# Optimization experiments

Hardware: AMD Instinct MI355X
Metric: run time of the kernel (lower is better)

Reference implementation:

```python
import jax, jax.numpy as jnp
import numpy as np

D = 1024      # input_dim == output_dim
H = 512       # expert_dim
E = 8         # num_experts
TOP_K = 2
LN_EPS = 1e-5


def setup_inputs() -> dict:
    key = jax.random.key(0)
    ks = jax.random.split(key, 9)
    s_in = 1.0 / np.sqrt(D)
    s_h = 1.0 / np.sqrt(H)
    return {
        "x": jax.random.normal(ks[0], (4, 4096, D), dtype=jnp.float32),
        "Wg": jax.random.uniform(ks[1], (D, E), jnp.float32, -s_in, s_in),
        "bg": jax.random.uniform(ks[2], (E,), jnp.float32, -s_in, s_in),
        "W1": jax.random.uniform(ks[3], (E, D, H), jnp.float32, -s_in, s_in),
        "b1": jax.random.uniform(ks[4], (E, H), jnp.float32, -s_in, s_in),
        "W2": jax.random.uniform(ks[5], (E, H, D), jnp.float32, -s_h, s_h),
        "b2": jax.random.uniform(ks[6], (E, D), jnp.float32, -s_h, s_h),
        "gamma": jnp.ones((E, D), jnp.float32),
        "beta": jnp.zeros((E, D), jnp.float32),
    }


def reference(x, Wg, bg, W1, b1, W2, b2, gamma, beta):
    B, S, _ = x.shape
    xf = x.reshape(-1, D)                                   # [T, D]
    T = xf.shape[0]

    # Router (eval mode: no noise). Softmax over the top-k logits only.
    gates = xf @ Wg + bg                                    # [T, E]
    topw, topi = jax.lax.top_k(gates, TOP_K)                # [T, K]
    topw = jax.nn.softmax(topw, axis=-1)
    # Dense combine weights [T, E] (top_k indices are distinct per token).
    combine = jnp.zeros((T, E), xf.dtype).at[
        jnp.arange(T)[:, None], topi].add(topw)

    # All experts applied densely, combined with sparse routing weights
    # (same math as the masked gather/scatter loop in the original).
    h = jax.nn.gelu(jnp.einsum('td,edh->teh', xf, W1) + b1,
                    approximate=False)                      # [T, E, H]
    y = jnp.einsum('teh,ehd->ted', h, W2) + b2 + xf[:, None, :]  # residual
    mu = jnp.mean(y, axis=-1, keepdims=True)
    var = jnp.mean(jnp.square(y - mu), axis=-1, keepdims=True)
    yn = (y - mu) * jax.lax.rsqrt(var + LN_EPS) * gamma + beta   # per-expert LN

    out = jnp.einsum('te,ted->td', combine, yn)             # weighted combine
    return out.reshape(B, S, D)
```

## Files before the change

kernel.cpp:

```cpp
#include <hip/hip_runtime.h>

#define TT 16384
#define DD 1024
#define HH 512
#define EE 8
#define NA (2*TT)
#define NBLK (NA/256)
#define SLOT_CAP (NA + EE*128)
#define MT_TILES (SLOT_CAP/128)

typedef __attribute__((ext_vector_type(4))) float f32x4;
typedef __attribute__((ext_vector_type(8))) short s16x8;

__device__ __forceinline__ unsigned short f2bf(float f) {
  unsigned u = __float_as_uint(f);
  return (unsigned short)((u + 0x7fffu + ((u >> 16) & 1u)) >> 16);
}
__device__ __forceinline__ float bf2f(unsigned short h) {
  return __uint_as_float(((unsigned)h) << 16);
}
__device__ __forceinline__ float gelu_fast(float v) {
  float z = 1.5957691216057308f * (v + 0.044715f * v * v * v);
  return v / (1.0f + __expf(-z));
}
__device__ __forceinline__ void gl_lds16(const unsigned short* g, unsigned short* l) {
  __builtin_amdgcn_global_load_lds(
      (const __attribute__((address_space(1))) void*)g,
      (__attribute__((address_space(3))) void*)l, 16, 0, 0);
}


__global__ __launch_bounds__(256) void k_transpose(
    const float* __restrict__ src, unsigned short* __restrict__ dst, int R, int C) {
  __shared__ float t[32][33];
  const int e = blockIdx.z;
  const float* S = src + (size_t)e * R * C;
  unsigned short* Dt = dst + (size_t)e * R * C;
  const int c0 = blockIdx.x * 32, r0 = blockIdx.y * 32;
  const int tx = threadIdx.x & 31, ty = threadIdx.x >> 5;
#pragma unroll
  for (int i = 0; i < 4; i++)
    t[ty + i * 8][tx] = S[(size_t)(r0 + ty + i * 8) * C + c0 + tx];
  __syncthreads();
#pragma unroll
  for (int i = 0; i < 4; i++)
    Dt[(size_t)(c0 + ty + i * 8) * R + r0 + tx] = f2bf(t[tx][ty + i * 8]);
}

__global__ __launch_bounds__(256) void k_wgt(const float* __restrict__ Wg,
                                             float* __restrict__ WgT) {
  __shared__ float lds[DD * EE];
  const int tid = threadIdx.x;
#pragma unroll
  for (int k = 0; k < 32; k++) lds[tid + 256 * k] = Wg[tid + 256 * k];
  __syncthreads();
#pragma unroll
  for (int k = 0; k < 32; k++) {
    int f = tid + 256 * k;
    WgT[f] = lds[(f & 1023) * 8 + (f >> 10)];
  }
}

__global__ __launch_bounds__(256) void k_router(
    const float* __restrict__ x, const float* __restrict__ WgT,
    const float* __restrict__ bg, int* __restrict__ tok_e,
    float* __restrict__ tok_w, unsigned short* __restrict__ xbf) {
  const int lane = threadIdx.x & 63, wid = threadIdx.x >> 6;
  const int t = blockIdx.x * 4 + wid;
  const float4* xr4 = (const float4*)(x + (size_t)t * DD);
  ushort4* xb4 = (ushort4*)(xbf + (size_t)t * DD);
  float4 xv[4];
#pragma unroll
  for (int i = 0; i < 4; i++) {
    xv[i] = xr4[i * 64 + lane];
    ushort4 h;
    h.x = f2bf(xv[i].x); h.y = f2bf(xv[i].y);
    h.z = f2bf(xv[i].z); h.w = f2bf(xv[i].w);
    xb4[i * 64 + lane] = h;
  }
  float g[8];
#pragma unroll
  for (int e = 0; e < 8; e++) {
    const float4* w4 = (const float4*)(WgT + (size_t)e * DD);
    float a = 0.f;
#pragma unroll
    for (int i = 0; i < 4; i++) {
      float4 wv = w4[i * 64 + lane];
      a += xv[i].x * wv.x + xv[i].y * wv.y + xv[i].z * wv.z + xv[i].w * wv.w;
    }
    g[e] = a;
  }
#pragma unroll
  for (int off = 32; off; off >>= 1)
#pragma unroll
    for (int e2 = 0; e2 < 8; e2++) g[e2] += __shfl_xor(g[e2], off);
  if (lane == 0) {
#pragma unroll
    for (int e2 = 0; e2 < 8; e2++) g[e2] += bg[e2];
    int e1 = 0;
#pragma unroll
    for (int e2 = 1; e2 < 8; e2++) if (g[e2] > g[e1]) e1 = e2;
    int es = (e1 == 0) ? 1 : 0;
#pragma unroll
    for (int e2 = 0; e2 < 8; e2++) if (e2 != e1 && g[e2] > g[es]) es = e2;
    float p2 = expf(g[es] - g[e1]);
    float invs = 1.0f / (1.0f + p2);
    tok_e[2 * t] = e1; tok_e[2 * t + 1] = es;
    tok_w[2 * t] = invs; tok_w[2 * t + 1] = p2 * invs;
  }
}

__global__ __launch_bounds__(256) void k_hist(
    const int* __restrict__ tok_e, int* __restrict__ lrank,
    int* __restrict__ blockHist) {
  __shared__ int waveCnt[4][8];
  __shared__ int waveBase[4][8];
  const int tid = threadIdx.x, lane = tid & 63, wid = tid >> 6;
  const int i = blockIdx.x * 256 + tid;
  const int e = tok_e[i];
  int rw = 0;
#pragma unroll
  for (int ex = 0; ex < 8; ex++) {
    unsigned long long m = __ballot(e == ex);
    if (e == ex) rw = __popcll(m & ((1ull << lane) - 1ull));
    if (lane == 0) waveCnt[wid][ex] = __popcll(m);
  }
  __syncthreads();
  if (tid < 8) {
    int a0 = waveCnt[0][tid], a1 = waveCnt[1][tid];
    int a2 = waveCnt[2][tid], a3 = waveCnt[3][tid];
    waveBase[0][tid] = 0;
    waveBase[1][tid] = a0;
    waveBase[2][tid] = a0 + a1;
    waveBase[3][tid] = a0 + a1 + a2;
    blockHist[blockIdx.x * 8 + tid] = a0 + a1 + a2 + a3;
  }
  __syncthreads();
  lrank[i] = waveBase[wid][e] + rw;
}

__global__ __launch_bounds__(512) void k_scan(
    const int* __restrict__ blockHist, int* __restrict__ blockBase,
    int* __restrict__ offs) {
  __shared__ int tot[8];
  const int e = threadIdx.x >> 6;
  const int lane = threadIdx.x & 63;
  int v0 = blockHist[lane * 8 + e];
  int v1 = blockHist[(64 + lane) * 8 + e];
  int s0 = v0, s1 = v1;
#pragma unroll
  for (int off = 1; off < 64; off <<= 1) {
    int u0 = __shfl_up(s0, off), u1 = __shfl_up(s1, off);
    if (lane >= off) { s0 += u0; s1 += u1; }
  }
  int t0 = __shfl(s0, 63);
  blockBase[lane * 8 + e] = s0 - v0;
  blockBase[(64 + lane) * 8 + e] = t0 + s1 - v1;
  if (lane == 63) tot[e] = t0 + s1;
  __syncthreads();
  if (threadIdx.x == 0) {
    int acc = 0;
    offs[0] = 0;
#pragma unroll
    for (int e2 = 0; e2 < 8; e2++) {
      acc += (tot[e2] + 127) & ~127;
      offs[e2 + 1] = acc;
    }
  }
}

__global__ __launch_bounds__(256) void k_slotinit(int* __restrict__ st, int n) {
  int i = blockIdx.x * 256 + threadIdx.x;
  if (i < n) st[i] = 0;
}

__global__ __launch_bounds__(256) void k_assign(
    const int* __restrict__ tok_e, const int* __restrict__ lrank,
    const int* __restrict__ blockBase, const int* __restrict__ offs,
    int* __restrict__ slot_token, int* __restrict__ token_slot) {
  const int i = blockIdx.x * 256 + threadIdx.x;
  const int e = tok_e[i];
  const int slot = offs[e] + blockBase[blockIdx.x * 8 + e] + lrank[i];
  slot_token[slot] = i >> 1;
  token_slot[i] = slot;
}

template <int K, bool GATHER, int EPI, int NOUT>
__global__ __launch_bounds__(256, 2) void k_gemm(
    const unsigned short* __restrict__ A, const unsigned short* __restrict__ Bt,
    const int* __restrict__ offs, const int* __restrict__ slot_token,
    const float* __restrict__ bias, const unsigned short* __restrict__ xres,
    unsigned short* __restrict__ Out) {
  __shared__ unsigned short sA[128 * 64];
  __shared__ unsigned short sB[128 * 64];
  constexpr int NCT = NOUT / 128;
  constexpr int NWG = MT_TILES * NCT;
  constexpr int CPX = NWG / 8;
  const int raw = blockIdx.x;
  const int bid = (raw & 7) * CPX + (raw >> 3);
  const int nt = bid % NCT;
  const int mt = bid / NCT;
  const int g0 = mt * 128;
  if (g0 >= offs[EE]) return;
  int e = 0;
  while (offs[e + 1] <= g0) ++e;
  const int col0 = nt * 128;
  const int tid = threadIdx.x;
  const int wid = tid >> 6;
  const int lane = tid & 63;

  const int swz = (((lane & 7) ^ ((lane >> 3) & 7))) * 8;
  const unsigned short* aptr[4];
  const unsigned short* bptr[4];
#pragma unroll
  for (int i = 0; i < 4; ++i) {
    int r = (i * 4 + wid) * 8 + (lane >> 3);
    int ar;
    if constexpr (GATHER) ar = slot_token[g0 + r];
    else ar = g0 + r;
    aptr[i] = A + (size_t)ar * K + swz;
    bptr[i] = Bt + ((size_t)e * NOUT + (col0 + r)) * K + swz;
  }

  f32x4 acc[4][4];
#pragma unroll
  for (int m = 0; m < 4; m++)
#pragma unroll
    for (int n = 0; n < 4; n++) acc[m][n] = (f32x4){0.f, 0.f, 0.f, 0.f};

  const int wr = (wid >> 1) * 64;
  const int wc = (wid & 1) * 64;
  const int lrow = lane & 15;
  const int khalf = lane >> 4;
  const int sx = lrow & 7;

  constexpr int NT = K / 64;
#pragma unroll 1
  for (int t = 0; t < NT; ++t) {
    const int k0 = t * 64;
#pragma unroll
    for (int i = 0; i < 4; ++i) {
      gl_lds16(aptr[i] + k0, sA + (i * 4 + wid) * 512);
      gl_lds16(bptr[i] + k0, sB + (i * 4 + wid) * 512);
    }
    __syncthreads();
#pragma unroll
    for (int kk = 0; kk < 2; ++kk) {
      const int so = ((kk * 4 + khalf) ^ sx) * 8;
      s16x8 af[4], bfr[4];
#pragma unroll
      for (int m = 0; m < 4; m++)
        af[m] = *(const s16x8*)(sA + (wr + m * 16 + lrow) * 64 + so);
#pragma unroll
      for (int n = 0; n < 4; n++)
        bfr[n] = *(const s16x8*)(sB + (wc + n * 16 + lrow) * 64 + so);
#pragma unroll
      for (int m = 0; m < 4; m++)
#pragma unroll
        for (int n = 0; n < 4; n++)
          acc[m][n] = __builtin_amdgcn_mfma_f32_16x16x32_bf16(af[m], bfr[n], acc[m][n], 0, 0, 0);
    }
    __syncthreads();
  }

  const float* bv = bias + (size_t)e * NOUT;
#pragma unroll
  for (int m = 0; m < 4; m++) {
    int r_base = wr + m * 16 + ((lane >> 4) << 2);
#pragma unroll
    for (int j = 0; j < 4; j++) {
      int gr = g0 + r_base + j;
      int tok = 0;
      if constexpr (EPI == 2) tok = slot_token[gr];
      size_t orow = (size_t)gr * NOUT;
#pragma unroll
      for (int n = 0; n < 4; n++) {
        int gc = col0 + wc + n * 16 + lrow;
        float v = acc[m][n][j] + bv[gc];
        if constexpr (EPI == 1) v = gelu_fast(v);
        if constexpr (EPI == 2) v += bf2f(xres[(size_t)tok * DD + gc]);
        Out[orow + gc] = f2bf(v);
      }
    }
  }
}

__global__ __launch_bounds__(256) void k_ln(
    const unsigned short* __restrict__ y, const int* __restrict__ token_slot,
    const int* __restrict__ tok_e, const float* __restrict__ tok_w,
    const float* __restrict__ gamma, const float* __restrict__ beta,
    float* __restrict__ out) {
  const int t = blockIdx.x;
  const int tid = threadIdx.x;
  const int lane = tid & 63, wid = tid >> 6;
  __shared__ float red[8];
  float o0 = 0, o1 = 0, o2 = 0, o3 = 0;
#pragma unroll
  for (int k = 0; k < 2; k++) {
    int slot = token_slot[2 * t + k];
    int e = tok_e[2 * t + k];
    float w = tok_w[2 * t + k];
    ushort4 raw = ((const ushort4*)(y + (size_t)slot * DD))[tid];
    float v0 = bf2f(raw.x), v1 = bf2f(raw.y), v2 = bf2f(raw.z), v3 = bf2f(raw.w);
    float s = v0 + v1 + v2 + v3;
    float s2 = v0 * v0 + v1 * v1 + v2 * v2 + v3 * v3;
#pragma unroll
    for (int off = 32; off; off >>= 1) {
      s += __shfl_xor(s, off);
      s2 += __shfl_xor(s2, off);
    }
    if (lane == 0) { red[wid] = s; red[4 + wid] = s2; }
    __syncthreads();
    s = red[0] + red[1] + red[2] + red[3];
    s2 = red[4] + red[5] + red[6] + red[7];
    float mu = s * (1.0f / 1024.0f);
    float var = s2 * (1.0f / 1024.0f) - mu * mu;
    float inv = rsqrtf(var + 1e-5f);
    float4 g4 = ((const float4*)(gamma + (size_t)e * DD))[tid];
    float4 b4 = ((const float4*)(beta + (size_t)e * DD))[tid];
    o0 += w * ((v0 - mu) * inv * g4.x + b4.x);
    o1 += w * ((v1 - mu) * inv * g4.y + b4.y);
    o2 += w * ((v2 - mu) * inv * g4.z + b4.z);
    o3 += w * ((v3 - mu) * inv * g4.w + b4.w);
    __syncthreads();
  }
  float4 r;
  r.x = o0; r.y = o1; r.z = o2; r.w = o3;
  ((float4*)(out + (size_t)t * DD))[tid] = r;
}


extern "C" void kernel_launch(void* const* d_in, const int* in_sizes, int n_in,
                              void* d_out, int out_size, void* d_ws, size_t ws_size,
                              hipStream_t stream) {
  const float* x = (const float*)d_in[0];
  const float* Wg = (const float*)d_in[1];
  const float* bg = (const float*)d_in[2];
  const float* W1 = (const float*)d_in[3];
  const float* b1 = (const float*)d_in[4];
  const float* W2 = (const float*)d_in[5];
  const float* b2 = (const float*)d_in[6];
  const float* gamma = (const float*)d_in[7];
  const float* beta = (const float*)d_in[8];
  float* out = (float*)d_out;

  char* ws = (char*)d_ws;
  size_t o = 0;
  auto take = [&](size_t b) -> void* {
    void* p = ws + o;
    o += (b + 255) & ~(size_t)255;
    return p;
  };
  int* offs = (int*)take((EE + 1) * 4);
  int* tok_e = (int*)take(NA * 4);
  int* lrank = (int*)take(NA * 4);
  int* token_slot = (int*)take(NA * 4);
  float* tok_w = (float*)take(NA * 4);
  int* blockHist = (int*)take(NBLK * EE * 4);
  int* blockBase = (int*)take(NBLK * EE * 4);
  int* slot_token = (int*)take(SLOT_CAP * 4);
  float* WgT = (float*)take((size_t)EE * DD * 4);
  unsigned short* xbf = (unsigned short*)take((size_t)TT * DD * 2);
  unsigned short* W1t = (unsigned short*)take((size_t)EE * HH * DD * 2);
  unsigned short* W2t = (unsigned short*)take((size_t)EE * DD * HH * 2);
  unsigned short* hbuf = (unsigned short*)take((size_t)SLOT_CAP * HH * 2);
  unsigned short* ybuf = (unsigned short*)take((size_t)SLOT_CAP * DD * 2);
  if (o > ws_size) return;

  k_transpose<<<dim3(HH / 32, DD / 32, EE), 256, 0, stream>>>(W1, W1t, DD, HH);
  k_transpose<<<dim3(DD / 32, HH / 32, EE), 256, 0, stream>>>(W2, W2t, HH, DD);
  k_wgt<<<1, 256, 0, stream>>>(Wg, WgT);
  k_router<<<TT / 4, 256, 0, stream>>>(x, WgT, bg, tok_e, tok_w, xbf);
  k_hist<<<NBLK, 256, 0, stream>>>(tok_e, lrank, blockHist);
  k_scan<<<1, 512, 0, stream>>>(blockHist, blockBase, offs);
  k_slotinit<<<(SLOT_CAP + 255) / 256, 256, 0, stream>>>(slot_token, SLOT_CAP);
  k_assign<<<NBLK, 256, 0, stream>>>(tok_e, lrank, blockBase, offs, slot_token,
                                     token_slot);
  k_gemm<1024, true, 1, 512><<<MT_TILES * (512 / 128), 256, 0, stream>>>(
      xbf, W1t, offs, slot_token, b1, nullptr, hbuf);
  k_gemm<512, false, 2, 1024><<<MT_TILES * (1024 / 128), 256, 0, stream>>>(
      hbuf, W2t, offs, slot_token, b2, xbf, ybuf);
  k_ln<<<TT, 256, 0, stream>>>(ybuf, token_slot, tok_e, tok_w, gamma, beta, out);
}
```

Before: 193.9 us.

## Use 256x256 double-buffered 8-wave GEMM tiles and move residual add into LN

Replaces the 128x128 single-buffered expert GEMM with a 256x256 tile kernel using 8 waves, double-buffered dynamic LDS (128KB), global-to-LDS prefetch of the next k-slice overlapped with MFMA, and setprio/sched barriers. Expert segments are padded to 256 rows to match the larger M tile. The residual x add moves from the second GEMM epilogue into the LayerNorm kernel. Larger tiles raise data reuse but cut the grid size and add more padding waste. The 128KB of LDS per block likely limits occupancy to one block per CU despite the launch bound.

```diff
diff --git a/kernel.cpp b/kernel.cpp
--- a/kernel.cpp
+++ b/kernel.cpp
@@ -6,8 +6,8 @@
 #define EE 8
 #define NA (2*TT)
 #define NBLK (NA/256)
-#define SLOT_CAP (NA + EE*128)
-#define MT_TILES (SLOT_CAP/128)
+#define SLOT_CAP (NA + EE*256)
+#define MT_TILES (SLOT_CAP/256)
 
 typedef __attribute__((ext_vector_type(4))) float f32x4;
 typedef __attribute__((ext_vector_type(8))) short s16x8;
@@ -163,7 +163,7 @@
     offs[0] = 0;
 #pragma unroll
     for (int e2 = 0; e2 < 8; e2++) {
-      acc += (tot[e2] + 127) & ~127;
+      acc += (tot[e2] + 255) & ~255;
       offs[e2 + 1] = acc;
     }
   }
@@ -186,99 +186,178 @@
 }
 
 template <int K, bool GATHER, int EPI, int NOUT>
-__global__ __launch_bounds__(256, 2) void k_gemm(
+__global__ __launch_bounds__(512, 2) void k_gemm8(
     const unsigned short* __restrict__ A, const unsigned short* __restrict__ Bt,
     const int* __restrict__ offs, const int* __restrict__ slot_token,
-    const float* __restrict__ bias, const unsigned short* __restrict__ xres,
-    unsigned short* __restrict__ Out) {
-  __shared__ unsigned short sA[128 * 64];
-  __shared__ unsigned short sB[128 * 64];
-  constexpr int NCT = NOUT / 128;
+    const float* __restrict__ bias, unsigned short* __restrict__ Out) {
+  extern __shared__ unsigned short lds[];
+  constexpr int NCT = NOUT / 256;
   constexpr int NWG = MT_TILES * NCT;
   constexpr int CPX = NWG / 8;
   const int raw = blockIdx.x;
   const int bid = (raw & 7) * CPX + (raw >> 3);
   const int nt = bid % NCT;
   const int mt = bid / NCT;
-  const int g0 = mt * 128;
+  const int g0 = mt * 256;
   if (g0 >= offs[EE]) return;
   int e = 0;
   while (offs[e + 1] <= g0) ++e;
-  const int col0 = nt * 128;
+  const int col0 = nt * 256;
   const int tid = threadIdx.x;
   const int wid = tid >> 6;
   const int lane = tid & 63;
-
-  const int swz = (((lane & 7) ^ ((lane >> 3) & 7))) * 8;
+  const int wm = wid >> 2, wn = wid & 3;
+
+  const int swz = ((lane & 7) ^ ((lane >> 3) & 7)) * 8;
   const unsigned short* aptr[4];
   const unsigned short* bptr[4];
 #pragma unroll
-  for (int i = 0; i < 4; ++i) {
-    int r = (i * 4 + wid) * 8 + (lane >> 3);
+  for (int j = 0; j < 4; ++j) {
+    int r = j * 64 + wid * 8 + (lane >> 3);
     int ar;
     if constexpr (GATHER) ar = slot_token[g0 + r];
     else ar = g0 + r;
-    aptr[i] = A + (size_t)ar * K + swz;
-    bptr[i] = Bt + ((size_t)e * NOUT + (col0 + r)) * K + swz;
-  }
-
-  f32x4 acc[4][4];
-#pragma unroll
-  for (int m = 0; m < 4; m++)
+    aptr[j] = A + (size_t)ar * K + swz;
+    bptr[j] = Bt + ((size_t)e * NOUT + (col0 + r)) * K + swz;
+  }
+  const int dstoff = wid * 512;
+
+  f32x4 acc[8][4];
+#pragma unroll
+  for (int m = 0; m < 8; m++)
 #pragma unroll
     for (int n = 0; n < 4; n++) acc[m][n] = (f32x4){0.f, 0.f, 0.f, 0.f};
 
-  const int wr = (wid >> 1) * 64;
-  const int wc = (wid & 1) * 64;
   const int lrow = lane & 15;
   const int khalf = lane >> 4;
   const int sx = lrow & 7;
 
+  auto stage = [&](int t) {
+    const int k0 = t * 64;
+    unsigned short* dA = lds + (t & 1) * 32768;
+    unsigned short* dB = dA + 16384;
+#pragma unroll
+    for (int j = 0; j < 4; ++j) gl_lds16(aptr[j] + k0, dA + j * 4096 + dstoff);
+#pragma unroll
+    for (int j = 0; j < 4; ++j) gl_lds16(bptr[j] + k0, dB + j * 4096 + dstoff);
+  };
+
+  stage(0);
+  asm volatile("s_waitcnt vmcnt(0)" ::: "memory");
+  __builtin_amdgcn_s_barrier();
+  __builtin_amdgcn_sched_barrier(0);
+
   constexpr int NT = K / 64;
 #pragma unroll 1
   for (int t = 0; t < NT; ++t) {
-    const int k0 = t * 64;
-#pragma unroll
-    for (int i = 0; i < 4; ++i) {
-      gl_lds16(aptr[i] + k0, sA + (i * 4 + wid) * 512);
-      gl_lds16(bptr[i] + k0, sB + (i * 4 + wid) * 512);
+    const unsigned short* sA = lds + (t & 1) * 32768;
+    const unsigned short* sB = sA + 16384;
+    s16x8 af[4][2], bf[2][2];
+
+#pragma unroll
+    for (int m4 = 0; m4 < 4; ++m4)
+#pragma unroll
+      for (int kk = 0; kk < 2; ++kk) {
+        int r = wm * 128 + m4 * 16 + lrow;
+        af[m4][kk] = *(const s16x8*)(sA + r * 64 + (((kk << 2) + khalf) ^ sx) * 8);
+      }
+#pragma unroll
+    for (int n2 = 0; n2 < 2; ++n2)
+#pragma unroll
+      for (int kk = 0; kk < 2; ++kk) {
+        int r = wn * 64 + n2 * 16 + lrow;
+        bf[n2][kk] = *(const s16x8*)(sB + r * 64 + (((kk << 2) + khalf) ^ sx) * 8);
+      }
+    if (t + 1 < NT) stage(t + 1);
+    __builtin_amdgcn_sched_barrier(0);
+    __builtin_amdgcn_s_barrier();
+    __builtin_amdgcn_s_setprio(1);
+#pragma unroll
+    for (int kk = 0; kk < 2; ++kk)
+#pragma unroll
+      for (int m4 = 0; m4 < 4; ++m4)
+#pragma unroll
+        for (int n2 = 0; n2 < 2; ++n2)
+          acc[m4][n2] = __builtin_amdgcn_mfma_f32_16x16x32_bf16(af[m4][kk], bf[n2][kk], acc[m4][n2], 0, 0, 0);
+    __builtin_amdgcn_s_setprio(0);
+
+#pragma unroll
+    for (int n2 = 0; n2 < 2; ++n2)
+#pragma unroll
+      for (int kk = 0; kk < 2; ++kk) {
+        int r = wn * 64 + 32 + n2 * 16 + lrow;
+        bf[n2][kk] = *(const s16x8*)(sB + r * 64 + (((kk << 2) + khalf) ^ sx) * 8);
+      }
+    __builtin_amdgcn_sched_barrier(0);
+    __builtin_amdgcn_s_barrier();
+    __builtin_amdgcn_s_setprio(1);
+#pragma unroll
+    for (int kk = 0; kk < 2; ++kk)
+#pragma unroll
+      for (int m4 = 0; m4 < 4; ++m4)
+#pragma unroll
+        for (int n2 = 0; n2 < 2; ++n2)
+          acc[m4][2 + n2] = __builtin_amdgcn_mfma_f32_16x16x32_bf16(af[m4][kk], bf[n2][kk], acc[m4][2 + n2], 0, 0, 0);
+    __builtin_amdgcn_s_setprio(0);
+
+#pragma unroll
+    for (int m4 = 0; m4 < 4; ++m4)
+#pragma unroll
+      for (int kk = 0; kk < 2; ++kk) {
+        int r = wm * 128 + 64 + m4 * 16 + lrow;
+        af[m4][kk] = *(const s16x8*)(sA + r * 64 + (((kk << 2) + khalf) ^ sx) * 8);
+      }
+    __builtin_amdgcn_sched_barrier(0);
+    __builtin_amdgcn_s_barrier();
+    __builtin_amdgcn_s_setprio(1);
+#pragma unroll
+    for (int kk = 0; kk < 2; ++kk)
+#pragma unroll
+      for (int m4 = 0; m4 < 4; ++m4)
+#pragma unroll
+        for (int n2 = 0; n2 < 2; ++n2)
+          acc[4 + m4][2 + n2] = __builtin_amdgcn_mfma_f32_16x16x32_bf16(af[m4][kk], bf[n2][kk], acc[4 + m4][2 + n2], 0, 0, 0);
+    __builtin_amdgcn_s_setprio(0);
+
+#pragma unroll
+    for (int n2 = 0; n2 < 2; ++n2)
+#pragma unroll
+      for (int kk = 0; kk < 2; ++kk) {
+        int r = wn * 64 + n2 * 16 + lrow;
+        bf[n2][kk] = *(const s16x8*)(sB + r * 64 + (((kk << 2) + khalf) ^ sx) * 8);
+      }
+    __builtin_amdgcn_sched_barrier(0);
+    __builtin_amdgcn_s_barrier();
+    __builtin_amdgcn_s_setprio(1);
+#pragma unroll
+    for (int kk = 0; kk < 2; ++kk)
+#pragma unroll
+      for (int m4 = 0; m4 < 4; ++m4)
+#pragma unroll
+        for (int n2 = 0; n2 < 2; ++n2)
+          acc[4 + m4][n2] = __builtin_amdgcn_mfma_f32_16x16x32_bf16(af[m4][kk], bf[n2][kk], acc[4 + m4][n2], 0, 0, 0);
+    __builtin_amdgcn_s_setprio(0);
+
+    if (t + 1 < NT) {
+      asm volatile("s_waitcnt vmcnt(0)" ::: "memory");
     }
-    __syncthreads();
-#pragma unroll
-    for (int kk = 0; kk < 2; ++kk) {
-      const int so = ((kk * 4 + khalf) ^ sx) * 8;
-      s16x8 af[4], bfr[4];
-#pragma unroll
-      for (int m = 0; m < 4; m++)
-        af[m] = *(const s16x8*)(sA + (wr + m * 16 + lrow) * 64 + so);
-#pragma unroll
-      for (int n = 0; n < 4; n++)
-        bfr[n] = *(const s16x8*)(sB + (wc + n * 16 + lrow) * 64 + so);
-#pragma unroll
-      for (int m = 0; m < 4; m++)
-#pragma unroll
-        for (int n = 0; n < 4; n++)
-          acc[m][n] = __builtin_amdgcn_mfma_f32_16x16x32_bf16(af[m], bfr[n], acc[m][n], 0, 0, 0);
-    }
-    __syncthreads();
+    __builtin_amdgcn_s_barrier();
+    __builtin_amdgcn_sched_barrier(0);
   }
 
   const float* bv = bias + (size_t)e * NOUT;
 #pragma unroll
-  for (int m = 0; m < 4; m++) {
-    int r_base = wr + m * 16 + ((lane >> 4) << 2);
-#pragma unroll
-    for (int j = 0; j < 4; j++) {
-      int gr = g0 + r_base + j;
-      int tok = 0;
-      if constexpr (EPI == 2) tok = slot_token[gr];
+  for (int m = 0; m < 8; ++m) {
+    int rb = wm * 128 + m * 16 + khalf * 4;
+#pragma unroll
+    for (int j = 0; j < 4; ++j) {
+      int gr = g0 + rb + j;
       size_t orow = (size_t)gr * NOUT;
 #pragma unroll
-      for (int n = 0; n < 4; n++) {
-        int gc = col0 + wc + n * 16 + lrow;
+      for (int n = 0; n < 4; ++n) {
+        int gc = col0 + wn * 64 + n * 16 + lrow;
         float v = acc[m][n][j] + bv[gc];
         if constexpr (EPI == 1) v = gelu_fast(v);
-        if constexpr (EPI == 2) v += bf2f(xres[(size_t)tok * DD + gc]);
         Out[orow + gc] = f2bf(v);
       }
     }
@@ -286,14 +365,16 @@
 }
 
 __global__ __launch_bounds__(256) void k_ln(
-    const unsigned short* __restrict__ y, const int* __restrict__ token_slot,
-    const int* __restrict__ tok_e, const float* __restrict__ tok_w,
-    const float* __restrict__ gamma, const float* __restrict__ beta,
-    float* __restrict__ out) {
+    const unsigned short* __restrict__ y, const unsigned short* __restrict__ xbf,
+    const int* __restrict__ token_slot, const int* __restrict__ tok_e,
+    const float* __restrict__ tok_w, const float* __restrict__ gamma,
+    const float* __restrict__ beta, float* __restrict__ out) {
   const int t = blockIdx.x;
   const int tid = threadIdx.x;
   const int lane = tid & 63, wid = tid >> 6;
   __shared__ float red[8];
+  ushort4 xu = ((const ushort4*)(xbf + (size_t)t * DD))[tid];
+  float x0 = bf2f(xu.x), x1 = bf2f(xu.y), x2 = bf2f(xu.z), x3 = bf2f(xu.w);
   float o0 = 0, o1 = 0, o2 = 0, o3 = 0;
 #pragma unroll
   for (int k = 0; k < 2; k++) {
@@ -301,7 +382,8 @@
     int e = tok_e[2 * t + k];
     float w = tok_w[2 * t + k];
     ushort4 raw = ((const ushort4*)(y + (size_t)slot * DD))[tid];
-    float v0 = bf2f(raw.x), v1 = bf2f(raw.y), v2 = bf2f(raw.z), v3 = bf2f(raw.w);
+    float v0 = bf2f(raw.x) + x0, v1 = bf2f(raw.y) + x1;
+    float v2 = bf2f(raw.z) + x2, v3 = bf2f(raw.w) + x3;
     float s = v0 + v1 + v2 + v3;
     float s2 = v0 * v0 + v1 * v1 + v2 * v2 + v3 * v3;
 #pragma unroll
@@ -367,6 +449,11 @@
   unsigned short* ybuf = (unsigned short*)take((size_t)SLOT_CAP * DD * 2);
   if (o > ws_size) return;
 
+  hipFuncSetAttribute((const void*)k_gemm8<1024, true, 1, 512>,
+                      hipFuncAttributeMaxDynamicSharedMemorySize, 131072);
+  hipFuncSetAttribute((const void*)k_gemm8<512, false, 2, 1024>,
+                      hipFuncAttributeMaxDynamicSharedMemorySize, 131072);
+
   k_transpose<<<dim3(HH / 32, DD / 32, EE), 256, 0, stream>>>(W1, W1t, DD, HH);
   k_transpose<<<dim3(DD / 32, HH / 32, EE), 256, 0, stream>>>(W2, W2t, HH, DD);
   k_wgt<<<1, 256, 0, stream>>>(Wg, WgT);
@@ -376,9 +463,10 @@
   k_slotinit<<<(SLOT_CAP + 255) / 256, 256, 0, stream>>>(slot_token, SLOT_CAP);
   k_assign<<<NBLK, 256, 0, stream>>>(tok_e, lrank, blockBase, offs, slot_token,
                                      token_slot);
-  k_gemm<1024, true, 1, 512><<<MT_TILES * (512 / 128), 256, 0, stream>>>(
-      xbf, W1t, offs, slot_token, b1, nullptr, hbuf);
-  k_gemm<512, false, 2, 1024><<<MT_TILES * (1024 / 128), 256, 0, stream>>>(
-      hbuf, W2t, offs, slot_token, b2, xbf, ybuf);
-  k_ln<<<TT, 256, 0, stream>>>(ybuf, token_slot, tok_e, tok_w, gamma, beta, out);
-}
+  k_gemm8<1024, true, 1, 512><<<MT_TILES * (512 / 256), 512, 131072, stream>>>(
+      xbf, W1t, offs, slot_token, b1, hbuf);
+  k_gemm8<512, false, 2, 1024><<<MT_TILES * (1024 / 256), 512, 131072, stream>>>(
+      hbuf, W2t, offs, slot_token, b2, ybuf);
+  k_ln<<<TT, 256, 0, stream>>>(ybuf, xbf, token_slot, tok_e, tok_w, gamma, beta,
+                               out);
+}
```

Measured after the change: 228.7 us. 17.9% more time.

## Move residual add into LN kernel, drop slot init, raise GEMM occupancy

Applied to the files above, without the earlier changes.

Moves the residual addition out of the second GEMM's epilogue (which gathered x rows per output row) into the LayerNorm kernel, which reads the token's x row once and adds it to both expert outputs. Removes the slot_token zero-init kernel by masking gathered indices into range so padded rows read some valid row. Raises GEMM launch bounds to 4 blocks per CU, trading register budget for occupancy with a risk of spills. Rounding differs slightly since y is stored to bf16 before the residual is added.

```diff
diff --git a/kernel.cpp b/kernel.cpp
--- a/kernel.cpp
+++ b/kernel.cpp
@@ -169,11 +169,6 @@
   }
 }
 
-__global__ __launch_bounds__(256) void k_slotinit(int* __restrict__ st, int n) {
-  int i = blockIdx.x * 256 + threadIdx.x;
-  if (i < n) st[i] = 0;
-}
-
 __global__ __launch_bounds__(256) void k_assign(
     const int* __restrict__ tok_e, const int* __restrict__ lrank,
     const int* __restrict__ blockBase, const int* __restrict__ offs,
@@ -186,11 +181,10 @@
 }
 
 template <int K, bool GATHER, int EPI, int NOUT>
-__global__ __launch_bounds__(256, 2) void k_gemm(
+__global__ __launch_bounds__(256, 4) void k_gemm(
     const unsigned short* __restrict__ A, const unsigned short* __restrict__ Bt,
     const int* __restrict__ offs, const int* __restrict__ slot_token,
-    const float* __restrict__ bias, const unsigned short* __restrict__ xres,
-    unsigned short* __restrict__ Out) {
+    const float* __restrict__ bias, unsigned short* __restrict__ Out) {
   __shared__ unsigned short sA[128 * 64];
   __shared__ unsigned short sB[128 * 64];
   constexpr int NCT = NOUT / 128;
@@ -216,7 +210,7 @@
   for (int i = 0; i < 4; ++i) {
     int r = (i * 4 + wid) * 8 + (lane >> 3);
     int ar;
-    if constexpr (GATHER) ar = slot_token[g0 + r];
+    if constexpr (GATHER) ar = slot_token[g0 + r] & (TT - 1);
     else ar = g0 + r;
     aptr[i] = A + (size_t)ar * K + swz;
     bptr[i] = Bt + ((size_t)e * NOUT + (col0 + r)) * K + swz;
@@ -266,19 +260,16 @@
   const float* bv = bias + (size_t)e * NOUT;
 #pragma unroll
   for (int m = 0; m < 4; m++) {
-    int r_base = wr + m * 16 + ((lane >> 4) << 2);
+    int r_base = wr + m * 16 + (khalf << 2);
 #pragma unroll
     for (int j = 0; j < 4; j++) {
       int gr = g0 + r_base + j;
-      int tok = 0;
-      if constexpr (EPI == 2) tok = slot_token[gr];
       size_t orow = (size_t)gr * NOUT;
 #pragma unroll
       for (int n = 0; n < 4; n++) {
         int gc = col0 + wc + n * 16 + lrow;
         float v = acc[m][n][j] + bv[gc];
         if constexpr (EPI == 1) v = gelu_fast(v);
-        if constexpr (EPI == 2) v += bf2f(xres[(size_t)tok * DD + gc]);
         Out[orow + gc] = f2bf(v);
       }
     }
@@ -286,14 +277,16 @@
 }
 
 __global__ __launch_bounds__(256) void k_ln(
-    const unsigned short* __restrict__ y, const int* __restrict__ token_slot,
-    const int* __restrict__ tok_e, const float* __restrict__ tok_w,
-    const float* __restrict__ gamma, const float* __restrict__ beta,
-    float* __restrict__ out) {
+    const unsigned short* __restrict__ y, const unsigned short* __restrict__ xbf,
+    const int* __restrict__ token_slot, const int* __restrict__ tok_e,
+    const float* __restrict__ tok_w, const float* __restrict__ gamma,
+    const float* __restrict__ beta, float* __restrict__ out) {
   const int t = blockIdx.x;
   const int tid = threadIdx.x;
   const int lane = tid & 63, wid = tid >> 6;
   __shared__ float red[8];
+  ushort4 xu = ((const ushort4*)(xbf + (size_t)t * DD))[tid];
+  float x0 = bf2f(xu.x), x1 = bf2f(xu.y), x2 = bf2f(xu.z), x3 = bf2f(xu.w);
   float o0 = 0, o1 = 0, o2 = 0, o3 = 0;
 #pragma unroll
   for (int k = 0; k < 2; k++) {
@@ -301,7 +294,8 @@
     int e = tok_e[2 * t + k];
     float w = tok_w[2 * t + k];
     ushort4 raw = ((const ushort4*)(y + (size_t)slot * DD))[tid];
-    float v0 = bf2f(raw.x), v1 = bf2f(raw.y), v2 = bf2f(raw.z), v3 = bf2f(raw.w);
+    float v0 = bf2f(raw.x) + x0, v1 = bf2f(raw.y) + x1;
+    float v2 = bf2f(raw.z) + x2, v3 = bf2f(raw.w) + x3;
     float s = v0 + v1 + v2 + v3;
     float s2 = v0 * v0 + v1 * v1 + v2 * v2 + v3 * v3;
 #pragma unroll
@@ -373,12 +367,12 @@
   k_router<<<TT / 4, 256, 0, stream>>>(x, WgT, bg, tok_e, tok_w, xbf);
   k_hist<<<NBLK, 256, 0, stream>>>(tok_e, lrank, blockHist);
   k_scan<<<1, 512, 0, stream>>>(blockHist, blockBase, offs);
-  k_slotinit<<<(SLOT_CAP + 255) / 256, 256, 0, stream>>>(slot_token, SLOT_CAP);
   k_assign<<<NBLK, 256, 0, stream>>>(tok_e, lrank, blockBase, offs, slot_token,
                                      token_slot);
   k_gemm<1024, true, 1, 512><<<MT_TILES * (512 / 128), 256, 0, stream>>>(
-      xbf, W1t, offs, slot_token, b1, nullptr, hbuf);
+      xbf, W1t, offs, slot_token, b1, hbuf);
   k_gemm<512, false, 2, 1024><<<MT_TILES * (1024 / 128), 256, 0, stream>>>(
-      hbuf, W2t, offs, slot_token, b2, xbf, ybuf);
-  k_ln<<<TT, 256, 0, stream>>>(ybuf, token_slot, tok_e, tok_w, gamma, beta, out);
-}
+      hbuf, W2t, offs, slot_token, b2, ybuf);
+  k_ln<<<TT, 256, 0, stream>>>(ybuf, xbf, token_slot, tok_e, tok_w, gamma, beta,
+                               out);
+}
```

Result: faster. 185.7 us (-4.2%).
